# Kernel optimization log

Measured on AMD Instinct MI355X. Metric: run time of the kernel, lower is better.

The kernel has to match this reference:

```python
import jax, jax.numpy as jnp
import numpy as np

B, S, D, DM, H, DH, DF, L, T = 4096, 64, 256, 512, 4, 64, 512, 6, 20


def mish(x):
    return x * jnp.tanh(jax.nn.softplus(x))


def layernorm(x, eps=1e-5):
    mu = jnp.mean(x, axis=-1, keepdims=True)
    var = jnp.var(x, axis=-1, keepdims=True)
    return (x - mu) * jax.lax.rsqrt(var + eps)


def setup_inputs() -> dict:
    key = jax.random.key(0)
    ks = iter(jax.random.split(key, 32))
    w = lambda *shape: jax.random.normal(next(ks), shape, dtype=jnp.float32) * 0.02
    inp = {
        'x_t': jax.random.normal(next(ks), (B, S, D), dtype=jnp.float32),
        't': jax.random.randint(next(ks), (B,), 0, T + 1),
        'backbone_latent': jax.random.normal(next(ks), (B, S, DM), dtype=jnp.float32),
        # timestep embedding
        'emb': w(T + 1, D),
        'te_w1': w(D, 4 * D), 'te_b1': jnp.zeros((4 * D,), jnp.float32),
        'te_w2': w(4 * D, D), 'te_b2': jnp.zeros((D,), jnp.float32),
        # cond projection
        'cp_w1': w(DM, D), 'cp_b1': jnp.zeros((D,), jnp.float32),
        'cp_w2': w(D, D), 'cp_b2': jnp.zeros((D,), jnp.float32),
        # stacked per-layer DiT block params [L, ...]
        'adaln_w': w(L, D, 6 * D), 'adaln_b': jnp.zeros((L, 6 * D), jnp.float32),
        'qkv_w': w(L, D, 3 * D), 'qkv_b': jnp.zeros((L, 3 * D), jnp.float32),
        'op_w': w(L, D, D), 'op_b': jnp.zeros((L, D), jnp.float32),
        'ffn_w1': w(L, D, DF), 'ffn_b1': jnp.zeros((L, DF), jnp.float32),
        'ffn_w2': w(L, DF, D), 'ffn_b2': jnp.zeros((L, D), jnp.float32),
        # final adaLN + projection (random here for nontrivial test, zero-init in original)
        'fa_w': w(D, 2 * D), 'fa_b': jnp.zeros((2 * D,), jnp.float32),
        'fp_w': w(D, D), 'fp_b': jnp.zeros((D,), jnp.float32),
    }
    return inp


def _forward(x_t, t, backbone_latent, emb, te_w1, te_b1, te_w2, te_b2,
             cp_w1, cp_b1, cp_w2, cp_b2, adaln_w, adaln_b, qkv_w, qkv_b,
             op_w, op_b, ffn_w1, ffn_b1, ffn_w2, ffn_b2, fa_w, fa_b, fp_w, fp_b):
    # conditioning vector c: [B, D]
    te = emb[t]                                   # [B, D]
    te = mish(te @ te_w1 + te_b1) @ te_w2 + te_b2
    cond = jnp.mean(backbone_latent, axis=1)      # [B, DM]
    cond = mish(cond @ cp_w1 + cp_b1) @ cp_w2 + cp_b2
    c = te + cond
    mc = mish(c)

    x = x_t
    for l in range(L):
        mod = (mc @ adaln_w[l] + adaln_b[l])[:, None, :]   # [B, 1, 6D]
        sh1, sc1, g1, sh2, sc2, g2 = jnp.split(mod, 6, axis=-1)
        # attention sub-block
        h = layernorm(x) * (1.0 + sc1) + sh1
        qkv = (h @ qkv_w[l] + qkv_b[l]).reshape(B, S, 3, H, DH)
        q = qkv[:, :, 0].transpose(0, 2, 1, 3)   # [B, H, S, DH]
        k = qkv[:, :, 1].transpose(0, 2, 1, 3)
        v = qkv[:, :, 2].transpose(0, 2, 1, 3)
        attn = jax.nn.softmax(jnp.einsum('bhsd,bhtd->bhst', q, k) * DH ** -0.5, axis=-1)
        h = jnp.einsum('bhst,bhtd->bhsd', attn, v).transpose(0, 2, 1, 3).reshape(B, S, D)
        h = h @ op_w[l] + op_b[l]
        x = x + g1 * h
        # FFN sub-block
        h = layernorm(x) * (1.0 + sc2) + sh2
        h = mish(h @ ffn_w1[l] + ffn_b1[l]) @ ffn_w2[l] + ffn_b2[l]
        x = x + g2 * h

    mod = (mc @ fa_w + fa_b)[:, None, :]
    shift, scale = jnp.split(mod, 2, axis=-1)
    x = layernorm(x) * (1.0 + scale) + shift
    return x @ fp_w + fp_b


def reference(x_t, t, backbone_latent, emb, te_w1, te_b1, te_w2, te_b2,
              cp_w1, cp_b1, cp_w2, cp_b2, adaln_w, adaln_b, qkv_w, qkv_b,
              op_w, op_b, ffn_w1, ffn_b1, ffn_w2, ffn_b2, fa_w, fa_b, fp_w, fp_b):
    return _forward(x_t, t, backbone_latent, emb, te_w1, te_b1, te_w2, te_b2,
                    cp_w1, cp_b1, cp_w2, cp_b2, adaln_w, adaln_b, qkv_w, qkv_b,
                    op_w, op_b, ffn_w1, ffn_b1, ffn_w2, ffn_b2, fa_w, fa_b, fp_w, fp_b)
```

## Files before the change

kernel.cpp:

```cpp
#include <hip/hip_runtime.h>

typedef unsigned short u16;
typedef float f32x4 __attribute__((ext_vector_type(4)));
typedef __bf16 bf16x8 __attribute__((ext_vector_type(8)));

__device__ __forceinline__ u16 f2b(float f) {
  unsigned u = __builtin_bit_cast(unsigned, f);
  u += 0x7FFF + ((u >> 16) & 1);
  return (u16)(u >> 16);
}

__device__ __forceinline__ float b2f(u16 v) {
  unsigned u = (unsigned)v << 16;
  return __builtin_bit_cast(float, u);
}

__device__ __forceinline__ f32x4 ld_bf4(const u16* p) {
  ushort4 v = *(const ushort4*)p;
  f32x4 r;
  r[0] = b2f(v.x); r[1] = b2f(v.y); r[2] = b2f(v.z); r[3] = b2f(v.w);
  return r;
}

__device__ __forceinline__ float mishf(float x) {
  float e = __expf(fminf(x, 20.f));
  float n = e * (e + 2.f);
  return x * __fdividef(n, n + 2.f);
}

__device__ __forceinline__ void gl_lds16(const void* g, void* l) {
  __builtin_amdgcn_global_load_lds((__attribute__((address_space(1))) void*)g,
                                   (__attribute__((address_space(3))) void*)l, 16, 0, 0);
}

__device__ __forceinline__ bf16x8 ldb8(const u16* p) {
  return __builtin_bit_cast(bf16x8, *(const uint4*)p);
}

__global__ __launch_bounds__(256)
void transpose_w(const float* __restrict__ in, u16* __restrict__ out, int K, int N) {
  __shared__ float tl[64][65];
  const long zoff = (long)blockIdx.z * K * N;
  in += zoff; out += zoff;
  const int n0 = blockIdx.x * 64, k0 = blockIdx.y * 64;
  const int c = threadIdx.x & 63, r0 = threadIdx.x >> 6;
#pragma unroll
  for (int i = 0; i < 16; ++i) {
    int r = i * 4 + r0;
    tl[r][c] = in[(long)(k0 + r) * N + n0 + c];
  }
  __syncthreads();
#pragma unroll
  for (int i = 0; i < 16; ++i) {
    int r = i * 4 + r0;
    out[(long)(n0 + r) * K + k0 + c] = f2b(tl[c][r]);
  }
}

__global__ __launch_bounds__(1024)
void te_table_kernel(const float* __restrict__ emb, const float* __restrict__ w1,
                     const float* __restrict__ b1, const float* __restrict__ w2,
                     const float* __restrict__ b2, float* __restrict__ table) {
  __shared__ float te[256];
  __shared__ float h1[1024];
  __shared__ float red[1024];
  const int tt = blockIdx.x, tid = threadIdx.x;
  if (tid < 256) te[tid] = emb[tt * 256 + tid];
  __syncthreads();
  float a = b1[tid];
#pragma unroll 8
  for (int k = 0; k < 256; ++k) a += te[k] * w1[k * 1024 + tid];
  h1[tid] = mishf(a);
  __syncthreads();
  const int j = tid & 255, kq = tid >> 8;
  float a2 = 0.f;
#pragma unroll 8
  for (int k = kq * 256; k < kq * 256 + 256; ++k) a2 += h1[k] * w2[k * 256 + j];
  red[tid] = a2;
  __syncthreads();
  if (tid < 256)
    table[tt * 256 + tid] = b2[tid] + red[tid] + red[tid + 256] + red[tid + 512] + red[tid + 768];
}

__global__ __launch_bounds__(256)
void cond_mean_kernel(const float* __restrict__ bb, u16* __restrict__ cond) {
  const int b = blockIdx.x, tid = threadIdx.x;
  const float* p = bb + (long)b * 64 * 512;
  for (int d = tid; d < 512; d += 256) {
    float s = 0.f;
#pragma unroll
    for (int t = 0; t < 64; ++t) s += p[t * 512 + d];
    cond[b * 512 + d] = f2b(s * (1.f / 64.f));
  }
}

__global__ __launch_bounds__(256)
void ln_mod(const float* __restrict__ x, const u16* __restrict__ modb,
            int mstride, int shoff, int scoff, u16* __restrict__ out) {
  const int lane = threadIdx.x & 63;
  const long row = (long)blockIdx.x * 4 + (threadIdx.x >> 6);
  const float4 xv = *(const float4*)(x + row * 256 + lane * 4);
  float s1 = xv.x + xv.y + xv.z + xv.w;
  float s2 = xv.x * xv.x + xv.y * xv.y + xv.z * xv.z + xv.w * xv.w;
#pragma unroll
  for (int m = 1; m < 64; m <<= 1) { s1 += __shfl_xor(s1, m); s2 += __shfl_xor(s2, m); }
  const float mean = s1 * (1.f / 256.f);
  float var = s2 * (1.f / 256.f) - mean * mean;
  const float rstd = rsqrtf(fmaxf(var, 0.f) + 1e-5f);
  const long b = row >> 6;
  const f32x4 sc = ld_bf4(modb + b * mstride + scoff + lane * 4);
  const f32x4 sh = ld_bf4(modb + b * mstride + shoff + lane * 4);
  ushort4 o;
  o.x = f2b((xv.x - mean) * rstd * (1.f + sc[0]) + sh[0]);
  o.y = f2b((xv.y - mean) * rstd * (1.f + sc[1]) + sh[1]);
  o.z = f2b((xv.z - mean) * rstd * (1.f + sc[2]) + sh[2]);
  o.w = f2b((xv.w - mean) * rstd * (1.f + sc[3]) + sh[3]);
  *(ushort4*)(out + row * 256 + lane * 4) = o;
}

template <int EPI>
__global__ __launch_bounds__(256)
void gemm_bt(const u16* __restrict__ A, const u16* __restrict__ Bt,
             const float* __restrict__ bias, void* __restrict__ outp,
             const int* __restrict__ tvec, const float* __restrict__ tetab,
             int M, int N, int K) {
  __shared__ __align__(16) u16 As[2][128 * 64];
  __shared__ __align__(16) u16 Bs[2][128 * 64];
  const int tid = threadIdx.x;
  const int lane = tid & 63;
  const int wave = tid >> 6;
  const int wr = (wave >> 1) << 6;
  const int wc = (wave & 1) << 6;
  const long tm = (long)blockIdx.y * 128;
  const long tn = (long)blockIdx.x * 128;
  const u16* Ag = A + tm * K;
  const u16* Bg = Bt + tn * K;
  f32x4 acc[4][4] = {};
  const int kcb = lane >> 4;
  const int swz = lane & 7;
  const int NT = K >> 6;

  auto stage = [&](int t, int buf) {
    const int k0 = t << 6;
#pragma unroll
    for (int i = 0; i < 4; ++i) {
      int c = tid + (i << 8);
      int r = c >> 3;
      int sch = (c & 7) ^ (r & 7);
      gl_lds16(Ag + (long)r * K + k0 + (sch << 3), &As[buf][c << 3]);
    }
#pragma unroll
    for (int i = 0; i < 4; ++i) {
      int c = tid + (i << 8);
      int r = c >> 3;
      int sch = (c & 7) ^ (r & 7);
      gl_lds16(Bg + (long)r * K + k0 + (sch << 3), &Bs[buf][c << 3]);
    }
  };

  stage(0, 0);
  __syncthreads();
  int cur = 0;
  for (int t = 0; t < NT; ++t) {
    if (t + 1 < NT) stage(t + 1, cur ^ 1);
#pragma unroll
    for (int kt = 0; kt < 2; ++kt) {
      const int ko = ((kt * 4 + kcb) ^ swz) << 3;
      bf16x8 av[4], bv[4];
#pragma unroll
      for (int mt = 0; mt < 4; ++mt)
        av[mt] = ldb8(&As[cur][(wr + mt * 16 + (lane & 15)) * 64 + ko]);
#pragma unroll
      for (int nt = 0; nt < 4; ++nt)
        bv[nt] = ldb8(&Bs[cur][(wc + nt * 16 + (lane & 15)) * 64 + ko]);
#pragma unroll
      for (int mt = 0; mt < 4; ++mt)
#pragma unroll
        for (int nt = 0; nt < 4; ++nt)
          acc[mt][nt] = __builtin_amdgcn_mfma_f32_16x16x32_bf16(bv[nt], av[mt], acc[mt][nt], 0, 0, 0);
    }
    __syncthreads();
    cur ^= 1;
  }
  const int rl = lane & 15;
  const int c4 = (lane >> 4) << 2;
  f32x4 b4[4];
#pragma unroll
  for (int nt = 0; nt < 4; ++nt)
    b4[nt] = *(const f32x4*)(bias + (int)tn + wc + nt * 16 + c4);
#pragma unroll
  for (int mt = 0; mt < 4; ++mt) {
    const unsigned row = (unsigned)(tm + wr + mt * 16 + rl);
    const unsigned rb = row * (unsigned)N;
#pragma unroll
    for (int nt = 0; nt < 4; ++nt) {
      const unsigned col = (unsigned)tn + wc + nt * 16 + c4;
      f32x4 v = acc[mt][nt] + b4[nt];
      if constexpr (EPI == 0) {
        ushort4 o;
        o.x = f2b(v[0]); o.y = f2b(v[1]); o.z = f2b(v[2]); o.w = f2b(v[3]);
        *(ushort4*)((u16*)outp + rb + col) = o;
      } else if constexpr (EPI == 1) {
        ushort4 o;
        o.x = f2b(mishf(v[0])); o.y = f2b(mishf(v[1]));
        o.z = f2b(mishf(v[2])); o.w = f2b(mishf(v[3]));
        *(ushort4*)((u16*)outp + rb + col) = o;
      } else if constexpr (EPI == 3) {
        *(f32x4*)((float*)outp + rb + col) = v;
      } else {
        const f32x4 te = *(const f32x4*)(tetab + tvec[row] * 256 + col);
        ushort4 o;
        o.x = f2b(mishf(v[0] + te[0])); o.y = f2b(mishf(v[1] + te[1]));
        o.z = f2b(mishf(v[2] + te[2])); o.w = f2b(mishf(v[3] + te[3]));
        *(ushort4*)((u16*)outp + rb + col) = o;
      }
    }
  }
}

template <int K, bool XF32>
__global__ __launch_bounds__(256)
void gemm_ln(const u16* __restrict__ A, const u16* __restrict__ Bt,
             const float* __restrict__ bias, const void* __restrict__ xin,
             const u16* __restrict__ gptr,
             const u16* __restrict__ lnsh, const u16* __restrict__ lnsc, int lnstride,
             u16* __restrict__ xout, u16* __restrict__ hout) {
  __shared__ __align__(16) u16 As[2][64 * 64];
  __shared__ __align__(16) u16 Bs[2][256 * 64];
  const int tid = threadIdx.x, lane = tid & 63, wave = tid >> 6;
  const int wc = wave << 6;
  const long tm = (long)blockIdx.x * 64;
  const u16* Ag = A + tm * K;
  const int rl = lane & 15;
  const int c4 = (lane >> 4) << 2;
  const int swz = lane & 7;
  const int NT = K >> 6;

  auto stage = [&](int t, int buf) {
    const int k0 = t << 6;
#pragma unroll
    for (int i = 0; i < 2; ++i) {
      int c = tid + (i << 8);
      int r = c >> 3;
      int sch = (c & 7) ^ (r & 7);
      gl_lds16(Ag + (long)r * K + k0 + (sch << 3), &As[buf][c << 3]);
    }
#pragma unroll
    for (int i = 0; i < 8; ++i) {
      int c = tid + (i << 8);
      int r = c >> 3;
      int sch = (c & 7) ^ (r & 7);
      gl_lds16(Bt + (long)r * K + k0 + (sch << 3), &Bs[buf][c << 3]);
    }
  };

  stage(0, 0);
  __syncthreads();

  f32x4 acc[4][4] = {};
  int cur = 0;
  for (int t = 0; t < NT; ++t) {
    if (t + 1 < NT) stage(t + 1, cur ^ 1);
#pragma unroll
    for (int kt = 0; kt < 2; ++kt) {
      const int ko = ((kt * 4 + (lane >> 4)) ^ swz) << 3;
      bf16x8 av[4], bv[4];
#pragma unroll
      for (int mt = 0; mt < 4; ++mt)
        av[mt] = ldb8(&As[cur][(mt * 16 + rl) * 64 + ko]);
#pragma unroll
      for (int nt = 0; nt < 4; ++nt)
        bv[nt] = ldb8(&Bs[cur][(wc + nt * 16 + rl) * 64 + ko]);
#pragma unroll
      for (int mt = 0; mt < 4; ++mt)
#pragma unroll
        for (int nt = 0; nt < 4; ++nt)
          acc[mt][nt] = __builtin_amdgcn_mfma_f32_16x16x32_bf16(bv[nt], av[mt], acc[mt][nt], 0, 0, 0);
    }
    __syncthreads();
    cur ^= 1;
  }

  const long b = blockIdx.x;
  float s1[4] = {}, s2[4] = {};
#pragma unroll
  for (int nt = 0; nt < 4; ++nt) {
    const int col = wc + nt * 16 + c4;
    const f32x4 b4 = *(const f32x4*)(bias + col);
    const f32x4 g4 = ld_bf4(gptr + b * 1536 + col);
#pragma unroll
    for (int mt = 0; mt < 4; ++mt) {
      const long row = tm + mt * 16 + rl;
      f32x4 x;
      if constexpr (XF32) x = *(const f32x4*)((const float*)xin + row * 256 + col);
      else x = ld_bf4((const u16*)xin + row * 256 + col);
      f32x4 xn = x + g4 * (acc[mt][nt] + b4);
      acc[mt][nt] = xn;
      s1[mt] += xn[0] + xn[1] + xn[2] + xn[3];
      s2[mt] += xn[0] * xn[0] + xn[1] * xn[1] + xn[2] * xn[2] + xn[3] * xn[3];
    }
  }
#pragma unroll
  for (int mt = 0; mt < 4; ++mt) {
    s1[mt] += __shfl_xor(s1[mt], 16); s1[mt] += __shfl_xor(s1[mt], 32);
    s2[mt] += __shfl_xor(s2[mt], 16); s2[mt] += __shfl_xor(s2[mt], 32);
  }
  float* st = (float*)&As[0][0];
  if (lane < 16) {
#pragma unroll
    for (int mt = 0; mt < 4; ++mt) {
      st[wave * 128 + mt * 16 + lane] = s1[mt];
      st[wave * 128 + 64 + mt * 16 + lane] = s2[mt];
    }
  }
  __syncthreads();
  float mean[4], rstd[4];
#pragma unroll
  for (int mt = 0; mt < 4; ++mt) {
    float a = 0.f, q = 0.f;
#pragma unroll
    for (int w2 = 0; w2 < 4; ++w2) {
      a += st[w2 * 128 + mt * 16 + rl];
      q += st[w2 * 128 + 64 + mt * 16 + rl];
    }
    mean[mt] = a * (1.f / 256.f);
    float var = q * (1.f / 256.f) - mean[mt] * mean[mt];
    rstd[mt] = rsqrtf(fmaxf(var, 0.f) + 1e-5f);
  }
#pragma unroll
  for (int nt = 0; nt < 4; ++nt) {
    const int col = wc + nt * 16 + c4;
    const f32x4 sc4 = ld_bf4(lnsc + b * lnstride + col);
    const f32x4 sh4 = ld_bf4(lnsh + b * lnstride + col);
#pragma unroll
    for (int mt = 0; mt < 4; ++mt) {
      const long row = tm + mt * 16 + rl;
      ushort4 xo;
      xo.x = f2b(acc[mt][nt][0]); xo.y = f2b(acc[mt][nt][1]);
      xo.z = f2b(acc[mt][nt][2]); xo.w = f2b(acc[mt][nt][3]);
      *(ushort4*)(xout + row * 256 + col) = xo;
      f32x4 h = (acc[mt][nt] - mean[mt]) * rstd[mt] * (1.f + sc4) + sh4;
      ushort4 o;
      o.x = f2b(h[0]); o.y = f2b(h[1]); o.z = f2b(h[2]); o.w = f2b(h[3]);
      *(ushort4*)(hout + row * 256 + col) = o;
    }
  }
}

__global__ __launch_bounds__(128)
void attn_kernel(const u16* __restrict__ qkv, u16* __restrict__ out) {
  __shared__ __align__(16) u16 vt_s[2][64 * 72];
  __shared__ __align__(16) u16 p_s[2][64 * 72];
  const int lane = threadIdx.x & 63;
  const int wave = threadIdx.x >> 6;
  const long b = blockIdx.x >> 1;
  const int h = ((blockIdx.x & 1) << 1) | wave;
  u16* vt = vt_s[wave];
  u16* pl = p_s[wave];
  const u16* base = qkv + b * (64 * 768);
#pragma unroll
  for (int it = 0; it < 8; ++it) {
    int chunk = it * 64 + lane;
    int t = chunk >> 3, dhb = (chunk & 7) << 3;
    union { uint4 u; u16 s[8]; } uv;
    uv.u = *(const uint4*)(base + t * 768 + 512 + h * 64 + dhb);
#pragma unroll
    for (int j = 0; j < 8; ++j) vt[(dhb + j) * 72 + t] = uv.s[j];
  }
  const u16* qb = base + h * 64;
  const u16* kb = base + 256 + h * 64;
  f32x4 sacc[4][4] = {};
#pragma unroll
  for (int kt = 0; kt < 2; ++kt) {
    bf16x8 qa[4], kv[4];
#pragma unroll
    for (int mt = 0; mt < 4; ++mt)
      qa[mt] = ldb8(qb + ((lane & 15) + mt * 16) * 768 + kt * 32 + ((lane >> 4) << 3));
#pragma unroll
    for (int nt = 0; nt < 4; ++nt)
      kv[nt] = ldb8(kb + ((lane & 15) + nt * 16) * 768 + kt * 32 + ((lane >> 4) << 3));
#pragma unroll
    for (int mt = 0; mt < 4; ++mt)
#pragma unroll
      for (int nt = 0; nt < 4; ++nt)
        sacc[mt][nt] = __builtin_amdgcn_mfma_f32_16x16x32_bf16(qa[mt], kv[nt], sacc[mt][nt], 0, 0, 0);
  }
  const float scale = 0.125f;
#pragma unroll
  for (int mt = 0; mt < 4; ++mt) {
#pragma unroll
    for (int r = 0; r < 4; ++r) {
      float mx = fmaxf(fmaxf(sacc[mt][0][r], sacc[mt][1][r]), fmaxf(sacc[mt][2][r], sacc[mt][3][r]));
#pragma unroll
      for (int m = 1; m <= 8; m <<= 1) mx = fmaxf(mx, __shfl_xor(mx, m));
      float p[4];
      float sum = 0.f;
#pragma unroll
      for (int nt = 0; nt < 4; ++nt) { p[nt] = __expf((sacc[mt][nt][r] - mx) * scale); sum += p[nt]; }
#pragma unroll
      for (int m = 1; m <= 8; m <<= 1) sum += __shfl_xor(sum, m);
      const float rinv = 1.f / sum;
      const int s = mt * 16 + ((lane >> 4) << 2) + r;
#pragma unroll
      for (int nt = 0; nt < 4; ++nt) pl[s * 72 + nt * 16 + (lane & 15)] = f2b(p[nt] * rinv);
    }
  }
  __syncthreads();
  f32x4 oacc[4][4] = {};
#pragma unroll
  for (int kt = 0; kt < 2; ++kt) {
    bf16x8 pa[4], vv[4];
#pragma unroll
    for (int mt = 0; mt < 4; ++mt)
      pa[mt] = ldb8(pl + ((lane & 15) + mt * 16) * 72 + kt * 32 + ((lane >> 4) << 3));
#pragma unroll
    for (int nt = 0; nt < 4; ++nt)
      vv[nt] = ldb8(vt + ((lane & 15) + nt * 16) * 72 + kt * 32 + ((lane >> 4) << 3));
#pragma unroll
    for (int mt = 0; mt < 4; ++mt)
#pragma unroll
      for (int nt = 0; nt < 4; ++nt)
        oacc[mt][nt] = __builtin_amdgcn_mfma_f32_16x16x32_bf16(vv[nt], pa[mt], oacc[mt][nt], 0, 0, 0);
  }
  u16* ob = out + b * (64 * 256) + h * 64;
#pragma unroll
  for (int mt = 0; mt < 4; ++mt)
#pragma unroll
    for (int nt = 0; nt < 4; ++nt) {
      const int s = mt * 16 + (lane & 15);
      const int d4 = nt * 16 + ((lane >> 4) << 2);
      ushort4 o;
      o.x = f2b(oacc[mt][nt][0]); o.y = f2b(oacc[mt][nt][1]);
      o.z = f2b(oacc[mt][nt][2]); o.w = f2b(oacc[mt][nt][3]);
      *(ushort4*)(ob + s * 256 + d4) = o;
    }
}

extern "C" void kernel_launch(void* const* d_in, const int* in_sizes, int n_in,
                              void* d_out, int out_size, void* d_ws, size_t ws_size,
                              hipStream_t stream) {
  (void)in_sizes; (void)n_in; (void)out_size; (void)ws_size;
  const int B = 4096, L = 6;
  const long BSr = (long)B * 64;

  const float* x_t = (const float*)d_in[0];
  const int* tvec = (const int*)d_in[1];
  const float* backbone = (const float*)d_in[2];
  const float* emb = (const float*)d_in[3];
  const float* te_w1 = (const float*)d_in[4];
  const float* te_b1 = (const float*)d_in[5];
  const float* te_w2 = (const float*)d_in[6];
  const float* te_b2 = (const float*)d_in[7];
  const float* cp_w1 = (const float*)d_in[8];
  const float* cp_b1 = (const float*)d_in[9];
  const float* cp_w2 = (const float*)d_in[10];
  const float* cp_b2 = (const float*)d_in[11];
  const float* adaln_w = (const float*)d_in[12];
  const float* adaln_b = (const float*)d_in[13];
  const float* qkv_w = (const float*)d_in[14];
  const float* qkv_b = (const float*)d_in[15];
  const float* op_w = (const float*)d_in[16];
  const float* op_b = (const float*)d_in[17];
  const float* ffn_w1 = (const float*)d_in[18];
  const float* ffn_b1 = (const float*)d_in[19];
  const float* ffn_w2 = (const float*)d_in[20];
  const float* ffn_b2 = (const float*)d_in[21];
  const float* fa_w = (const float*)d_in[22];
  const float* fa_b = (const float*)d_in[23];
  const float* fp_w = (const float*)d_in[24];
  const float* fp_b = (const float*)d_in[25];

  char* w = (char*)d_ws;
  auto alloc = [&](size_t bytes) { char* p = w; w += (bytes + 255) & ~(size_t)255; return p; };
  u16* WT_cp1 = (u16*)alloc(256L * 512 * 2);
  u16* WT_cp2 = (u16*)alloc(256L * 256 * 2);
  u16* WT_adaln = (u16*)alloc(6L * 1536 * 256 * 2);
  u16* WT_qkv = (u16*)alloc(6L * 768 * 256 * 2);
  u16* WT_op = (u16*)alloc(6L * 256 * 256 * 2);
  u16* WT_f1 = (u16*)alloc(6L * 512 * 256 * 2);
  u16* WT_f2 = (u16*)alloc(6L * 256 * 512 * 2);
  u16* WT_fa = (u16*)alloc(512L * 256 * 2);
  u16* WT_fp = (u16*)alloc(256L * 256 * 2);
  float* te_tab = (float*)alloc(21L * 256 * 4);
  u16* cond = (u16*)alloc(4096L * 512 * 2);
  u16* c1 = (u16*)alloc(4096L * 256 * 2);
  u16* mc = (u16*)alloc(4096L * 256 * 2);
  u16* modb6 = (u16*)alloc(6L * 4096 * 1536 * 2);
  u16* famod = (u16*)alloc(4096L * 512 * 2);
  u16* hbuf = (u16*)alloc(BSr * 256 * 2);
  u16* qkvbuf = (u16*)alloc(BSr * 768 * 2);
  u16* xbuf = (u16*)d_out;

  transpose_w<<<dim3(4, 8, 1), 256, 0, stream>>>(cp_w1, WT_cp1, 512, 256);
  transpose_w<<<dim3(4, 4, 1), 256, 0, stream>>>(cp_w2, WT_cp2, 256, 256);
  transpose_w<<<dim3(24, 4, 6), 256, 0, stream>>>(adaln_w, WT_adaln, 256, 1536);
  transpose_w<<<dim3(12, 4, 6), 256, 0, stream>>>(qkv_w, WT_qkv, 256, 768);
  transpose_w<<<dim3(4, 4, 6), 256, 0, stream>>>(op_w, WT_op, 256, 256);
  transpose_w<<<dim3(8, 4, 6), 256, 0, stream>>>(ffn_w1, WT_f1, 256, 512);
  transpose_w<<<dim3(4, 8, 6), 256, 0, stream>>>(ffn_w2, WT_f2, 512, 256);
  transpose_w<<<dim3(8, 4, 1), 256, 0, stream>>>(fa_w, WT_fa, 256, 512);
  transpose_w<<<dim3(4, 4, 1), 256, 0, stream>>>(fp_w, WT_fp, 256, 256);

  te_table_kernel<<<21, 1024, 0, stream>>>(emb, te_w1, te_b1, te_w2, te_b2, te_tab);
  cond_mean_kernel<<<4096, 256, 0, stream>>>(backbone, cond);

  gemm_bt<1><<<dim3(2, 32), 256, 0, stream>>>(cond, WT_cp1, cp_b1, c1, nullptr, nullptr, 4096, 256, 512);
  gemm_bt<4><<<dim3(2, 32), 256, 0, stream>>>(c1, WT_cp2, cp_b2, mc, tvec, te_tab, 4096, 256, 256);
  gemm_bt<0><<<dim3(4, 32), 256, 0, stream>>>(mc, WT_fa, fa_b, famod, nullptr, nullptr, 4096, 512, 256);
  for (int l = 0; l < L; ++l)
    gemm_bt<0><<<dim3(12, 32), 256, 0, stream>>>(mc, WT_adaln + (long)l * 1536 * 256, adaln_b + l * 1536,
                                                 modb6 + (long)l * 4096 * 1536, nullptr, nullptr, 4096, 1536, 256);

  ln_mod<<<BSr / 4, 256, 0, stream>>>(x_t, modb6, 1536, 0, 256, hbuf);

  for (int l = 0; l < L; ++l) {
    const u16* mb = modb6 + (long)l * 4096 * 1536;
    gemm_bt<0><<<dim3(6, BSr / 128), 256, 0, stream>>>(hbuf, WT_qkv + (long)l * 768 * 256, qkv_b + l * 768,
                                                       qkvbuf, nullptr, nullptr, (int)BSr, 768, 256);
    attn_kernel<<<B * 2, 128, 0, stream>>>(qkvbuf, hbuf);
    if (l == 0)
      gemm_ln<256, true><<<BSr / 64, 256, 0, stream>>>(hbuf, WT_op, op_b, x_t, mb + 512,
                                                       mb + 768, mb + 1024, 1536, xbuf, hbuf);
    else
      gemm_ln<256, false><<<BSr / 64, 256, 0, stream>>>(hbuf, WT_op + (long)l * 256 * 256, op_b + l * 256,
                                                        xbuf, mb + 512, mb + 768, mb + 1024, 1536, xbuf, hbuf);
    gemm_bt<1><<<dim3(4, BSr / 128), 256, 0, stream>>>(hbuf, WT_f1 + (long)l * 512 * 256, ffn_b1 + l * 512,
                                                       qkvbuf, nullptr, nullptr, (int)BSr, 512, 256);
    const u16* nsh = (l < 5) ? (modb6 + (long)(l + 1) * 4096 * 1536) : famod;
    const u16* nsc = (l < 5) ? (modb6 + (long)(l + 1) * 4096 * 1536 + 256) : (famod + 256);
    const int nstride = (l < 5) ? 1536 : 512;
    gemm_ln<512, false><<<BSr / 64, 256, 0, stream>>>(qkvbuf, WT_f2 + (long)l * 256 * 512, ffn_b2 + l * 256,
                                                      xbuf, mb + 1280, nsh, nsc, nstride, xbuf, hbuf);
  }
  gemm_bt<3><<<dim3(2, BSr / 128), 256, 0, stream>>>(hbuf, WT_fp, fp_b, d_out, nullptr, nullptr, (int)BSr, 256, 256);
}
```

Measured before the change: 6.803 ms.

## Fuse FFN up-projection, Mish, down-projection and residual LayerNorm into one kernel

Replaces the two FFN launches (gemm_bt with Mish, then gemm_ln) with a single ffn_fused kernel per 64-row batch element. The kernel keeps the 64x512 Mish intermediate in LDS, streams W1 and W2 tiles through a double-buffered LDS stage, and applies the residual, gate and next-layer LayerNorm modulation in its epilogue. This removes the global write and read of the [B*S,512] intermediate and one launch per layer. In exchange it uses about 128KB of LDS per block, which allows only one block per CU, and each block reloads the full weights, which may limit occupancy and latency hiding.

```diff
diff --git a/kernel.cpp b/kernel.cpp
--- a/kernel.cpp
+++ b/kernel.cpp
@@ -340,6 +340,187 @@
       xo.z = f2b(acc[mt][nt][2]); xo.w = f2b(acc[mt][nt][3]);
       *(ushort4*)(xout + row * 256 + col) = xo;
       f32x4 h = (acc[mt][nt] - mean[mt]) * rstd[mt] * (1.f + sc4) + sh4;
+      ushort4 o;
+      o.x = f2b(h[0]); o.y = f2b(h[1]); o.z = f2b(h[2]); o.w = f2b(h[3]);
+      *(ushort4*)(hout + row * 256 + col) = o;
+    }
+  }
+}
+
+__global__ __launch_bounds__(512)
+void ffn_fused(const u16* __restrict__ xln, const u16* __restrict__ W1t,
+               const float* __restrict__ b1, const u16* __restrict__ W2t,
+               const float* __restrict__ b2, const u16* __restrict__ xres,
+               const u16* __restrict__ gptr,
+               const u16* __restrict__ lnsh, const u16* __restrict__ lnsc, int lnstride,
+               u16* __restrict__ xout, u16* __restrict__ hout) {
+  __shared__ __align__(16) u16 Ax[64 * 256];
+  __shared__ __align__(16) u16 Ws[2][256 * 64];
+  __shared__ __align__(16) u16 H1[64 * 512];
+  const int tid = threadIdx.x, lane = tid & 63, wave = tid >> 6;
+  const long b = blockIdx.x;
+  const int rl = lane & 15;
+  const int c4 = (lane >> 4) << 2;
+  const int kq = lane >> 4;
+
+  {
+    const u16* src = xln + b * (64 * 256);
+#pragma unroll
+    for (int i = 0; i < 4; ++i) {
+      int c = tid + (i << 9);
+      int r = c >> 5, cc = c & 31;
+      int sch = (cc & ~7) | ((cc & 7) ^ (r & 7));
+      gl_lds16(src + r * 256 + (sch << 3), &Ax[c << 3]);
+    }
+  }
+  auto stageW = [&](const u16* Wsrc, int Kw, int R0, int k0, int buf) {
+#pragma unroll
+    for (int i = 0; i < 4; ++i) {
+      int c = tid + (i << 9);
+      int r = c >> 3;
+      int sch = (c & 7) ^ (r & 7);
+      gl_lds16(Wsrc + (long)(R0 + r) * Kw + k0 + (sch << 3), &Ws[buf][c << 3]);
+    }
+  };
+  stageW(W1t, 256, 0, 0, 0);
+  __syncthreads();
+
+  int cur = 0;
+  for (int nh = 0; nh < 2; ++nh) {
+    f32x4 acc[4][2] = {};
+    for (int t = 0; t < 4; ++t) {
+      int s = nh * 4 + t;
+      if (s < 7) stageW(W1t, 256, ((s + 1) >> 2) * 256, ((s + 1) & 3) * 64, cur ^ 1);
+      else stageW(W2t, 512, 0, 0, cur ^ 1);
+#pragma unroll
+      for (int kt = 0; kt < 2; ++kt) {
+        bf16x8 av[4], bv[2];
+#pragma unroll
+        for (int mt = 0; mt < 4; ++mt) {
+          int r = mt * 16 + rl;
+          int kc = t * 8 + kt * 4 + kq;
+          int slot = (kc & ~7) | ((kc & 7) ^ (r & 7));
+          av[mt] = ldb8(&Ax[r * 256 + (slot << 3)]);
+        }
+#pragma unroll
+        for (int nf = 0; nf < 2; ++nf) {
+          int wr_ = wave * 32 + nf * 16 + rl;
+          int slot = (kt * 4 + kq) ^ (wr_ & 7);
+          bv[nf] = ldb8(&Ws[cur][wr_ * 64 + (slot << 3)]);
+        }
+#pragma unroll
+        for (int mt = 0; mt < 4; ++mt)
+#pragma unroll
+          for (int nf = 0; nf < 2; ++nf)
+            acc[mt][nf] = __builtin_amdgcn_mfma_f32_16x16x32_bf16(bv[nf], av[mt], acc[mt][nf], 0, 0, 0);
+      }
+      __syncthreads();
+      cur ^= 1;
+    }
+#pragma unroll
+    for (int nf = 0; nf < 2; ++nf) {
+      const int col = nh * 256 + wave * 32 + nf * 16 + c4;
+      const f32x4 bb = *(const f32x4*)(b1 + col);
+      const int c8 = col >> 3;
+      const int sub = (col & 7) << 1;
+#pragma unroll
+      for (int mt = 0; mt < 4; ++mt) {
+        const int r = mt * 16 + rl;
+        f32x4 v = acc[mt][nf] + bb;
+        ushort4 o;
+        o.x = f2b(mishf(v[0])); o.y = f2b(mishf(v[1]));
+        o.z = f2b(mishf(v[2])); o.w = f2b(mishf(v[3]));
+        int slot = (c8 & ~7) | ((c8 & 7) ^ (r & 7));
+        *(ushort4*)((char*)H1 + r * 1024 + (slot << 4) + sub) = o;
+      }
+    }
+  }
+  __syncthreads();
+
+  f32x4 acc[4][2] = {};
+  for (int t = 0; t < 8; ++t) {
+    if (t < 7) stageW(W2t, 512, 0, (t + 1) * 64, cur ^ 1);
+#pragma unroll
+    for (int kt = 0; kt < 2; ++kt) {
+      bf16x8 av[4], bv[2];
+#pragma unroll
+      for (int mt = 0; mt < 4; ++mt) {
+        int r = mt * 16 + rl;
+        int kc = t * 8 + kt * 4 + kq;
+        int slot = (kc & ~7) | ((kc & 7) ^ (r & 7));
+        av[mt] = ldb8((const u16*)((const char*)H1 + r * 1024 + (slot << 4)));
+      }
+#pragma unroll
+      for (int nf = 0; nf < 2; ++nf) {
+        int wr_ = wave * 32 + nf * 16 + rl;
+        int slot = (kt * 4 + kq) ^ (wr_ & 7);
+        bv[nf] = ldb8(&Ws[cur][wr_ * 64 + (slot << 3)]);
+      }
+#pragma unroll
+      for (int mt = 0; mt < 4; ++mt)
+#pragma unroll
+        for (int nf = 0; nf < 2; ++nf)
+          acc[mt][nf] = __builtin_amdgcn_mfma_f32_16x16x32_bf16(bv[nf], av[mt], acc[mt][nf], 0, 0, 0);
+    }
+    __syncthreads();
+    cur ^= 1;
+  }
+  float s1[4] = {}, s2[4] = {};
+#pragma unroll
+  for (int nf = 0; nf < 2; ++nf) {
+    const int col = wave * 32 + nf * 16 + c4;
+    const f32x4 bb = *(const f32x4*)(b2 + col);
+    const f32x4 g4 = ld_bf4(gptr + b * 1536 + col);
+#pragma unroll
+    for (int mt = 0; mt < 4; ++mt) {
+      const long row = b * 64 + mt * 16 + rl;
+      f32x4 x = ld_bf4(xres + row * 256 + col);
+      f32x4 xn = x + g4 * (acc[mt][nf] + bb);
+      acc[mt][nf] = xn;
+      s1[mt] += xn[0] + xn[1] + xn[2] + xn[3];
+      s2[mt] += xn[0] * xn[0] + xn[1] * xn[1] + xn[2] * xn[2] + xn[3] * xn[3];
+    }
+  }
+#pragma unroll
+  for (int mt = 0; mt < 4; ++mt) {
+    s1[mt] += __shfl_xor(s1[mt], 16); s1[mt] += __shfl_xor(s1[mt], 32);
+    s2[mt] += __shfl_xor(s2[mt], 16); s2[mt] += __shfl_xor(s2[mt], 32);
+  }
+  float* st = (float*)&Ax[0];
+  if (lane < 16) {
+#pragma unroll
+    for (int mt = 0; mt < 4; ++mt) {
+      st[wave * 128 + mt * 16 + lane] = s1[mt];
+      st[wave * 128 + 64 + mt * 16 + lane] = s2[mt];
+    }
+  }
+  __syncthreads();
+  float mean[4], rstd[4];
+#pragma unroll
+  for (int mt = 0; mt < 4; ++mt) {
+    float a = 0.f, q = 0.f;
+#pragma unroll
+    for (int w2 = 0; w2 < 8; ++w2) {
+      a += st[w2 * 128 + mt * 16 + rl];
+      q += st[w2 * 128 + 64 + mt * 16 + rl];
+    }
+    mean[mt] = a * (1.f / 256.f);
+    float var = q * (1.f / 256.f) - mean[mt] * mean[mt];
+    rstd[mt] = rsqrtf(fmaxf(var, 0.f) + 1e-5f);
+  }
+#pragma unroll
+  for (int nf = 0; nf < 2; ++nf) {
+    const int col = wave * 32 + nf * 16 + c4;
+    const f32x4 sc4 = ld_bf4(lnsc + b * lnstride + col);
+    const f32x4 sh4 = ld_bf4(lnsh + b * lnstride + col);
+#pragma unroll
+    for (int mt = 0; mt < 4; ++mt) {
+      const long row = b * 64 + mt * 16 + rl;
+      ushort4 xo;
+      xo.x = f2b(acc[mt][nf][0]); xo.y = f2b(acc[mt][nf][1]);
+      xo.z = f2b(acc[mt][nf][2]); xo.w = f2b(acc[mt][nf][3]);
+      *(ushort4*)(xout + row * 256 + col) = xo;
+      f32x4 h = (acc[mt][nf] - mean[mt]) * rstd[mt] * (1.f + sc4) + sh4;
       ushort4 o;
       o.x = f2b(h[0]); o.y = f2b(h[1]); o.z = f2b(h[2]); o.w = f2b(h[3]);
       *(ushort4*)(hout + row * 256 + col) = o;
@@ -524,13 +705,12 @@
     else
       gemm_ln<256, false><<<BSr / 64, 256, 0, stream>>>(hbuf, WT_op + (long)l * 256 * 256, op_b + l * 256,
                                                         xbuf, mb + 512, mb + 768, mb + 1024, 1536, xbuf, hbuf);
-    gemm_bt<1><<<dim3(4, BSr / 128), 256, 0, stream>>>(hbuf, WT_f1 + (long)l * 512 * 256, ffn_b1 + l * 512,
-                                                       qkvbuf, nullptr, nullptr, (int)BSr, 512, 256);
     const u16* nsh = (l < 5) ? (modb6 + (long)(l + 1) * 4096 * 1536) : famod;
     const u16* nsc = (l < 5) ? (modb6 + (long)(l + 1) * 4096 * 1536 + 256) : (famod + 256);
     const int nstride = (l < 5) ? 1536 : 512;
-    gemm_ln<512, false><<<BSr / 64, 256, 0, stream>>>(qkvbuf, WT_f2 + (long)l * 256 * 512, ffn_b2 + l * 256,
-                                                      xbuf, mb + 1280, nsh, nsc, nstride, xbuf, hbuf);
+    ffn_fused<<<B, 512, 0, stream>>>(hbuf, WT_f1 + (long)l * 512 * 256, ffn_b1 + l * 512,
+                                     WT_f2 + (long)l * 256 * 512, ffn_b2 + l * 256,
+                                     xbuf, mb + 1280, nsh, nsc, nstride, xbuf, hbuf);
   }
   gemm_bt<3><<<dim3(2, BSr / 128), 256, 0, stream>>>(hbuf, WT_fp, fp_b, d_out, nullptr, nullptr, (int)BSr, 256, 256);
 }
```

New measurement: 6.485 ms. 1.05x faster.
